# Performance work log

Measured on AMD Instinct MI355X. Metric: run time of the kernel, lower is better.

Reference implementation:

```python
import jax, jax.numpy as jnp
import numpy as np

# DynamicMaskHead config (CondLaneHead defaults, head_layers=3, channels=64)
N, INS_PER_IMG, C, H, W = 4, 8, 64, 160, 256
CIN = C + 2  # coords concatenated
L1, L2, L3 = (C + 2) * C, C * C, C * 1  # weight_nums = [4224, 4096, 64]
B1, B2, B3 = C, C, 1                     # bias_nums   = [64, 64, 1]
NUM_PARAMS = L1 + L2 + L3 + B1 + B2 + B3  # 8513
MASK_BIAS_SHIFT = 2.19  # subtracted from last bias when is_mask=True


def setup_inputs() -> dict:
    key = jax.random.key(0)
    k1, k2 = jax.random.split(key)
    x = jax.random.normal(k1, (N, C, H, W), dtype=jnp.float32)
    mask_head_params = jax.random.normal(k2, (N * INS_PER_IMG, NUM_PARAMS), dtype=jnp.float32) * 0.05
    num_ins = np.full((N,), INS_PER_IMG, dtype=np.int32)  # static per-image instance counts
    return {"x": x, "mask_head_params": mask_head_params, "num_ins": num_ins}


def _locations(h, w, dtype):
    # compute_locations with stride=1: +stride//2 == +0; original normalization
    # (locations[:0], locations[:1]) is a no-op slice, so coords stay unnormalized.
    loc_x = jnp.broadcast_to(jnp.arange(w, dtype=dtype)[None, :], (h, w))
    loc_y = jnp.broadcast_to(jnp.arange(h, dtype=dtype)[:, None], (h, w))
    return jnp.stack([loc_x, loc_y], axis=0)  # [2, H, W]


def reference(x, mask_head_params, num_ins):
    n, _, h, w = x.shape
    loc = _locations(h, w, x.dtype)
    xa = jnp.concatenate([jnp.broadcast_to(loc[None], (n, 2, h, w)), x], axis=1)  # [N, 66, H, W]

    # replicate each image's features per instance (grouped-conv input)
    img_idx = np.repeat(np.arange(n), np.asarray(num_ins))  # static
    num_insts = img_idx.shape[0]
    feats = xa[img_idx].reshape(num_insts, CIN, h * w)  # [I, 66, L]

    # parse_dynamic_params: split flat params into per-instance 1x1 conv weights/biases
    splits = jnp.split(mask_head_params, np.cumsum([L1, L2, L3, B1, B2]), axis=1)
    w0 = splits[0].reshape(num_insts, C, CIN)
    w1 = splits[1].reshape(num_insts, C, C)
    w2 = splits[2].reshape(num_insts, 1, C)
    b0 = splits[3]
    b1 = splits[4]
    b2 = splits[5] - MASK_BIAS_SHIFT  # is_mask=True

    # grouped 1x1 convs == per-instance small matmuls (batched GEMM)
    hdn = jax.nn.relu(jnp.einsum('ioc,icl->iol', w0, feats) + b0[:, :, None])
    hdn = jax.nn.relu(jnp.einsum('ioc,icl->iol', w1, hdn) + b1[:, :, None])
    out = jnp.einsum('ioc,icl->iol', w2, hdn) + b2[:, :, None]  # [I, 1, L]
    return out.reshape(1, num_insts, h, w)
```

## Files before the change

kernel.cpp:

```cpp
#include <hip/hip_runtime.h>
#include <hip/hip_bf16.h>


#define NP 8513
#define HW 40960
#define ISTRIDE 18432
#define OFF_W1 8192
#define OFF_VEC 16384

typedef __attribute__((ext_vector_type(8))) short bf16x8;
typedef __attribute__((ext_vector_type(4))) float f32x4;

__device__ inline unsigned short f2bf(float f) {
  union { float f; unsigned u; } v; v.f = f;
  unsigned r = v.u + 0x7fffu + ((v.u >> 16) & 1u);
  return (unsigned short)(r >> 16);
}
__device__ inline unsigned pk2(float a, float b) {
  __hip_bfloat162 h = __float22bfloat162_rn(float2{a, b});
  union { __hip_bfloat162 h; unsigned u; } v; v.h = h;
  return v.u;
}
__device__ inline void gld16(const void* g, void* l) {
  __builtin_amdgcn_global_load_lds(
      (const __attribute__((address_space(1))) unsigned*)g,
      (__attribute__((address_space(3))) unsigned*)l, 16, 0, 0);
}

__global__ void condlane_prep(const float* __restrict__ params,
                              char* __restrict__ ws) {
  const int inst = blockIdx.x >> 1, part = blockIdx.x & 1;
  const float* __restrict__ p = params + inst * NP;
  char* base = ws + inst * ISTRIDE;
  const int t = threadIdx.x;
  if (part == 0) {
    unsigned short* dst = (unsigned short*)base;
#pragma unroll
    for (int it = 0; it < 16; it++) {
      const int e = it * 256 + t;
      const int frag = e >> 9, lane = (e >> 3) & 63, j = e & 7;
      const int m = (frag >> 1) * 16 + (lane & 15);
      const int k = (frag & 1) * 32 + ((lane >> 4) << 3) + j;
      dst[e] = f2bf(p[m * 66 + 2 + k]);
    }
  } else {
    unsigned short* dst = (unsigned short*)(base + OFF_W1);
#pragma unroll
    for (int it = 0; it < 16; it++) {
      const int e = it * 256 + t;
      const int frag = e >> 9, lane = (e >> 3) & 63, j = e & 7;
      const int m = (frag >> 1) * 16 + (lane & 15);
      const int k = (frag & 1) * 32 + ((lane >> 4) << 3) + j;
      dst[e] = f2bf(p[4224 + m * 64 + k]);
    }
    float* vec = (float*)(base + OFF_VEC);
    if (t < 64) {
      vec[t]       = p[8384 + t];
      vec[64 + t]  = p[t * 66];
      vec[128 + t] = p[t * 66 + 1];
      vec[192 + t] = p[8448 + t];
      vec[256 + t] = p[8320 + t];
    } else if (t == 64) vec[320] = p[8512] - 2.19f;
  }
}

__global__ __launch_bounds__(256, 3) void condlane_main(
    const float* __restrict__ x, const char* __restrict__ ws,
    float* __restrict__ out) {
  __shared__ __align__(16) char smem[53248];
  const int img = blockIdx.y, bx = blockIdx.x;
  const int tid = threadIdx.x, lane = tid & 63, wave = tid >> 6;
  const int col = lane & 15, q = lane >> 4, sw = col & 7;
  const char* const wsb = ws + img * 8 * ISTRIDE;

  auto dma = [&](int i, char* buf) {
    const char* src = wsb + i * ISTRIDE;
#pragma unroll
    for (int u = 0; u < 4; u++) {
      const int off = (wave * 4 + u) * 1024;
      gld16(src + off + lane * 16, buf + off);
    }
    if (wave < 2) {
      const int off = OFF_VEC + wave * 1024;
      gld16(src + off + lane * 16, buf + off);
    }
  };
  dma(0, smem);

  bf16x8 bfr[2][2];
  {
    const float* gx = x + img * 64 * HW + bx * 128 + wave * 32;
#pragma unroll
    for (int nt = 0; nt < 2; nt++)
#pragma unroll
      for (int ks = 0; ks < 2; ks++) {
        float f[8];
#pragma unroll
        for (int j = 0; j < 8; j++)
          f[j] = gx[(ks * 32 + q * 8 + j) * HW + nt * 16 + col];
        union { bf16x8 v; unsigned d[4]; } u;
#pragma unroll
        for (int jj = 0; jj < 4; jj++) u.d[jj] = pk2(f[2 * jj], f[2 * jj + 1]);
        bfr[nt][ks] = u.v;
      }
  }
  __syncthreads();

  const float fyv = (float)(bx >> 1);
  const float fx0 = (float)((bx & 1) * 128 + wave * 32 + col);
  unsigned short* const hwv = (unsigned short*)(smem + 36864) + wave * 2048;
  float* const outb = out + img * 8 * HW + bx * 128 + wave * 32;

  for (int i = 0; i < 8; i++) {
    char* const wb = smem + (i & 1) * ISTRIDE;
    if (i < 7) dma(i + 1, smem + ((i + 1) & 1) * ISTRIDE);
    const float* const vec = (const float*)(wb + OFF_VEC);

    f32x4 acc[4][2];
#pragma unroll
    for (int mt = 0; mt < 4; mt++) {
      const int ro = mt * 16 + q * 4;
      const f32x4 b0v = *(const f32x4*)(vec + ro);
      const f32x4 wxv = *(const f32x4*)(vec + 64 + ro);
      const f32x4 wyv = *(const f32x4*)(vec + 128 + ro);
      const f32x4 byv = b0v + wyv * fyv;
      acc[mt][0] = byv + wxv * fx0;
      acc[mt][1] = byv + wxv * (fx0 + 16.0f);
    }
#pragma unroll
    for (int mt = 0; mt < 4; mt++) {
      const bf16x8 a0 = *(const bf16x8*)(wb + (mt * 2 + 0) * 1024 + lane * 16);
      const bf16x8 a1 = *(const bf16x8*)(wb + (mt * 2 + 1) * 1024 + lane * 16);
#pragma unroll
      for (int nt = 0; nt < 2; nt++) {
        f32x4 c = __builtin_amdgcn_mfma_f32_16x16x32_bf16(a0, bfr[nt][0],
                                                          acc[mt][nt], 0, 0, 0);
        acc[mt][nt] = __builtin_amdgcn_mfma_f32_16x16x32_bf16(a1, bfr[nt][1],
                                                              c, 0, 0, 0);
      }
    }
#pragma unroll
    for (int nt = 0; nt < 2; nt++)
#pragma unroll
      for (int mt = 0; mt < 4; mt++) {
        const f32x4 v = acc[mt][nt];
        uint2 dd;
        dd.x = pk2(fmaxf(v.x, 0.f), fmaxf(v.y, 0.f));
        dd.y = pk2(fmaxf(v.z, 0.f), fmaxf(v.w, 0.f));
        const int kb = (mt * 2 + (q >> 1)) ^ sw;
        *(uint2*)(hwv + nt * 1024 + col * 64 + (kb << 3) + ((q & 1) << 2)) = dd;
      }
    bf16x8 hbf[2][2];
#pragma unroll
    for (int nt = 0; nt < 2; nt++)
#pragma unroll
      for (int ks = 0; ks < 2; ks++)
        hbf[nt][ks] = *(const bf16x8*)(hwv + nt * 1024 + col * 64 +
                                       (((ks * 4 + q) ^ sw) << 3));

    float s0 = 0.f, s1 = 0.f;
#pragma unroll
    for (int mt = 0; mt < 4; mt++) {
      const bf16x8 a0 = *(const bf16x8*)(wb + OFF_W1 + (mt * 2 + 0) * 1024 + lane * 16);
      const bf16x8 a1 = *(const bf16x8*)(wb + OFF_W1 + (mt * 2 + 1) * 1024 + lane * 16);
      const int ro = mt * 16 + q * 4;
      const f32x4 cb  = *(const f32x4*)(vec + 192 + ro);
      const f32x4 w2v = *(const f32x4*)(vec + 256 + ro);
      f32x4 c0 = __builtin_amdgcn_mfma_f32_16x16x32_bf16(a0, hbf[0][0], cb, 0, 0, 0);
      const f32x4 v0 = __builtin_amdgcn_mfma_f32_16x16x32_bf16(a1, hbf[0][1], c0, 0, 0, 0);
      f32x4 c1 = __builtin_amdgcn_mfma_f32_16x16x32_bf16(a0, hbf[1][0], cb, 0, 0, 0);
      const f32x4 v1 = __builtin_amdgcn_mfma_f32_16x16x32_bf16(a1, hbf[1][1], c1, 0, 0, 0);
      s0 += w2v.x * fmaxf(v0.x, 0.f) + w2v.y * fmaxf(v0.y, 0.f) +
            w2v.z * fmaxf(v0.z, 0.f) + w2v.w * fmaxf(v0.w, 0.f);
      s1 += w2v.x * fmaxf(v1.x, 0.f) + w2v.y * fmaxf(v1.y, 0.f) +
            w2v.z * fmaxf(v1.z, 0.f) + w2v.w * fmaxf(v1.w, 0.f);
    }
    const float b2i = vec[320];
    s0 += __shfl_xor(s0, 16, 64); s0 += __shfl_xor(s0, 32, 64);
    s1 += __shfl_xor(s1, 16, 64); s1 += __shfl_xor(s1, 32, 64);
    if (lane < 32)
      outb[i * HW + q * 16 + col] = (q ? s1 : s0) + b2i;

    if (i < 7) __syncthreads();
  }
}

extern "C" void kernel_launch(void* const* d_in, const int* in_sizes, int n_in,
                              void* d_out, int out_size, void* d_ws, size_t ws_size,
                              hipStream_t stream) {
  const float* x      = (const float*)d_in[0];
  const float* params = (const float*)d_in[1];
  float* out = (float*)d_out;

  condlane_prep<<<64, 256, 0, stream>>>(params, (char*)d_ws);
  condlane_main<<<dim3(320, 4), 256, 0, stream>>>(x, (const char*)d_ws, out);
}
```

Measured before the change: 113.2 us.

## Fold layer-0 bias and coords into an extra MFMA, read W1 from global

```diff
diff --git a/kernel.cpp b/kernel.cpp
--- a/kernel.cpp
+++ b/kernel.cpp
@@ -4,9 +4,10 @@
 
 #define NP 8513
 #define HW 40960
-#define ISTRIDE 18432
-#define OFF_W1 8192
-#define OFF_VEC 16384
+#define ISTRIDE 21504
+#define OFF_VEC 12288
+#define OFF_W1 13312
+#define DMABYTES 13312
 
 typedef __attribute__((ext_vector_type(8))) short bf16x8;
 typedef __attribute__((ext_vector_type(4))) float f32x4;
@@ -15,6 +16,10 @@
   union { float f; unsigned u; } v; v.f = f;
   unsigned r = v.u + 0x7fffu + ((v.u >> 16) & 1u);
   return (unsigned short)(r >> 16);
+}
+__device__ inline float bf2f(unsigned short b) {
+  union { unsigned u; float f; } v; v.u = ((unsigned)b) << 16;
+  return v.f;
 }
 __device__ inline unsigned pk2(float a, float b) {
   __hip_bfloat162 h = __float22bfloat162_rn(float2{a, b});
@@ -36,13 +41,27 @@
   if (part == 0) {
     unsigned short* dst = (unsigned short*)base;
 #pragma unroll
-    for (int it = 0; it < 16; it++) {
+    for (int it = 0; it < 24; it++) {
       const int e = it * 256 + t;
       const int frag = e >> 9, lane = (e >> 3) & 63, j = e & 7;
-      const int m = (frag >> 1) * 16 + (lane & 15);
-      const int k = (frag & 1) * 32 + ((lane >> 4) << 3) + j;
-      dst[e] = f2bf(p[m * 66 + 2 + k]);
-    }
+      const int mt = frag / 3, kst = frag % 3;
+      const int m = mt * 16 + (lane & 15);
+      const int kl = ((lane >> 4) << 3) + j;
+      unsigned short bv;
+      if (kst < 2) bv = f2bf(p[m * 66 + 2 + kst * 32 + kl]);
+      else if (kl == 0) bv = f2bf(p[8384 + m]);
+      else if (kl == 1) bv = f2bf(p[m * 66]);
+      else if (kl == 2) { float w = p[m * 66];     bv = f2bf(w - bf2f(f2bf(w))); }
+      else if (kl == 3) bv = f2bf(p[m * 66 + 1]);
+      else if (kl == 4) { float w = p[m * 66 + 1]; bv = f2bf(w - bf2f(f2bf(w))); }
+      else if (kl == 5) { float w = p[8384 + m];   bv = f2bf(w - bf2f(f2bf(w))); }
+      else bv = 0;
+      dst[e] = bv;
+    }
+    float* vec = (float*)(base + OFF_VEC);
+    if (t < 64) { vec[t] = p[8448 + t]; vec[64 + t] = p[8320 + t]; }
+    else if (t == 64) vec[128] = p[8512] - 2.19f;
+    else if (t >= 65 && t < 128) vec[64 + t] = 0.f;
   } else {
     unsigned short* dst = (unsigned short*)(base + OFF_W1);
 #pragma unroll
@@ -53,21 +72,13 @@
       const int k = (frag & 1) * 32 + ((lane >> 4) << 3) + j;
       dst[e] = f2bf(p[4224 + m * 64 + k]);
     }
-    float* vec = (float*)(base + OFF_VEC);
-    if (t < 64) {
-      vec[t]       = p[8384 + t];
-      vec[64 + t]  = p[t * 66];
-      vec[128 + t] = p[t * 66 + 1];
-      vec[192 + t] = p[8448 + t];
-      vec[256 + t] = p[8320 + t];
-    } else if (t == 64) vec[320] = p[8512] - 2.19f;
   }
 }
 
 __global__ __launch_bounds__(256, 3) void condlane_main(
     const float* __restrict__ x, const char* __restrict__ ws,
     float* __restrict__ out) {
-  __shared__ __align__(16) char smem[53248];
+  __shared__ __align__(16) char smem[34816];
   const int img = blockIdx.y, bx = blockIdx.x;
   const int tid = threadIdx.x, lane = tid & 63, wave = tid >> 6;
   const int col = lane & 15, q = lane >> 4, sw = col & 7;
@@ -76,14 +87,12 @@
   auto dma = [&](int i, char* buf) {
     const char* src = wsb + i * ISTRIDE;
 #pragma unroll
-    for (int u = 0; u < 4; u++) {
-      const int off = (wave * 4 + u) * 1024;
+    for (int u = 0; u < 3; u++) {
+      const int off = (wave * 3 + u) * 1024;
       gld16(src + off + lane * 16, buf + off);
     }
-    if (wave < 2) {
-      const int off = OFF_VEC + wave * 1024;
-      gld16(src + off + lane * 16, buf + off);
-    }
+    if (wave == 3 && lane < 48)
+      gld16(src + OFF_VEC + lane * 16, buf + OFF_VEC);
   };
   dma(0, smem);
 
@@ -104,43 +113,52 @@
         bfr[nt][ks] = u.v;
       }
   }
+  bf16x8 baug[2];
+  {
+    const unsigned short fyb = f2bf((float)(bx >> 1));
+#pragma unroll
+    for (int nt = 0; nt < 2; nt++) {
+      const unsigned short fxb =
+          f2bf((float)((bx & 1) * 128 + wave * 32 + nt * 16 + col));
+      union { bf16x8 v; unsigned short s[8]; } u;
+      u.s[0] = (q == 0) ? (unsigned short)0x3F80 : (unsigned short)0;
+      u.s[1] = (q == 0) ? fxb : (unsigned short)0;
+      u.s[2] = u.s[1];
+      u.s[3] = (q == 0) ? fyb : (unsigned short)0;
+      u.s[4] = u.s[3];
+      u.s[5] = u.s[0];
+      u.s[6] = 0; u.s[7] = 0;
+      baug[nt] = u.v;
+    }
+  }
   __syncthreads();
 
-  const float fyv = (float)(bx >> 1);
-  const float fx0 = (float)((bx & 1) * 128 + wave * 32 + col);
-  unsigned short* const hwv = (unsigned short*)(smem + 36864) + wave * 2048;
+  unsigned short* const hwv = (unsigned short*)(smem + 26624) + wave * 1024;
   float* const outb = out + img * 8 * HW + bx * 128 + wave * 32;
+  const f32x4 z4 = {0.f, 0.f, 0.f, 0.f};
 
   for (int i = 0; i < 8; i++) {
-    char* const wb = smem + (i & 1) * ISTRIDE;
-    if (i < 7) dma(i + 1, smem + ((i + 1) & 1) * ISTRIDE);
+    char* const wb = smem + (i & 1) * DMABYTES;
+    if (i < 7) dma(i + 1, smem + ((i + 1) & 1) * DMABYTES);
     const float* const vec = (const float*)(wb + OFF_VEC);
+    const char* const w1g = wsb + i * ISTRIDE + OFF_W1;
 
     f32x4 acc[4][2];
 #pragma unroll
     for (int mt = 0; mt < 4; mt++) {
-      const int ro = mt * 16 + q * 4;
-      const f32x4 b0v = *(const f32x4*)(vec + ro);
-      const f32x4 wxv = *(const f32x4*)(vec + 64 + ro);
-      const f32x4 wyv = *(const f32x4*)(vec + 128 + ro);
-      const f32x4 byv = b0v + wyv * fyv;
-      acc[mt][0] = byv + wxv * fx0;
-      acc[mt][1] = byv + wxv * (fx0 + 16.0f);
-    }
-#pragma unroll
-    for (int mt = 0; mt < 4; mt++) {
-      const bf16x8 a0 = *(const bf16x8*)(wb + (mt * 2 + 0) * 1024 + lane * 16);
-      const bf16x8 a1 = *(const bf16x8*)(wb + (mt * 2 + 1) * 1024 + lane * 16);
+      const bf16x8 a0 = *(const bf16x8*)(wb + (mt * 3 + 0) * 1024 + lane * 16);
+      const bf16x8 a1 = *(const bf16x8*)(wb + (mt * 3 + 1) * 1024 + lane * 16);
+      const bf16x8 a2 = *(const bf16x8*)(wb + (mt * 3 + 2) * 1024 + lane * 16);
 #pragma unroll
       for (int nt = 0; nt < 2; nt++) {
-        f32x4 c = __builtin_amdgcn_mfma_f32_16x16x32_bf16(a0, bfr[nt][0],
-                                                          acc[mt][nt], 0, 0, 0);
-        acc[mt][nt] = __builtin_amdgcn_mfma_f32_16x16x32_bf16(a1, bfr[nt][1],
-                                                              c, 0, 0, 0);
+        f32x4 c = __builtin_amdgcn_mfma_f32_16x16x32_bf16(a0, bfr[nt][0], z4, 0, 0, 0);
+        c = __builtin_amdgcn_mfma_f32_16x16x32_bf16(a1, bfr[nt][1], c, 0, 0, 0);
+        acc[mt][nt] = __builtin_amdgcn_mfma_f32_16x16x32_bf16(a2, baug[nt], c, 0, 0, 0);
       }
     }
-#pragma unroll
-    for (int nt = 0; nt < 2; nt++)
+    bf16x8 hbf[2][2];
+#pragma unroll
+    for (int nt = 0; nt < 2; nt++) {
 #pragma unroll
       for (int mt = 0; mt < 4; mt++) {
         const f32x4 v = acc[mt][nt];
@@ -148,24 +166,20 @@
         dd.x = pk2(fmaxf(v.x, 0.f), fmaxf(v.y, 0.f));
         dd.y = pk2(fmaxf(v.z, 0.f), fmaxf(v.w, 0.f));
         const int kb = (mt * 2 + (q >> 1)) ^ sw;
-        *(uint2*)(hwv + nt * 1024 + col * 64 + (kb << 3) + ((q & 1) << 2)) = dd;
+        *(uint2*)(hwv + col * 64 + (kb << 3) + ((q & 1) << 2)) = dd;
       }
-    bf16x8 hbf[2][2];
-#pragma unroll
-    for (int nt = 0; nt < 2; nt++)
 #pragma unroll
       for (int ks = 0; ks < 2; ks++)
-        hbf[nt][ks] = *(const bf16x8*)(hwv + nt * 1024 + col * 64 +
-                                       (((ks * 4 + q) ^ sw) << 3));
-
+        hbf[nt][ks] = *(const bf16x8*)(hwv + col * 64 + (((ks * 4 + q) ^ sw) << 3));
+    }
     float s0 = 0.f, s1 = 0.f;
 #pragma unroll
     for (int mt = 0; mt < 4; mt++) {
-      const bf16x8 a0 = *(const bf16x8*)(wb + OFF_W1 + (mt * 2 + 0) * 1024 + lane * 16);
-      const bf16x8 a1 = *(const bf16x8*)(wb + OFF_W1 + (mt * 2 + 1) * 1024 + lane * 16);
+      const bf16x8 a0 = *(const bf16x8*)(w1g + (mt * 2 + 0) * 1024 + lane * 16);
+      const bf16x8 a1 = *(const bf16x8*)(w1g + (mt * 2 + 1) * 1024 + lane * 16);
       const int ro = mt * 16 + q * 4;
-      const f32x4 cb  = *(const f32x4*)(vec + 192 + ro);
-      const f32x4 w2v = *(const f32x4*)(vec + 256 + ro);
+      const f32x4 cb  = *(const f32x4*)(vec + ro);
+      const f32x4 w2v = *(const f32x4*)(vec + 64 + ro);
       f32x4 c0 = __builtin_amdgcn_mfma_f32_16x16x32_bf16(a0, hbf[0][0], cb, 0, 0, 0);
       const f32x4 v0 = __builtin_amdgcn_mfma_f32_16x16x32_bf16(a1, hbf[0][1], c0, 0, 0, 0);
       f32x4 c1 = __builtin_amdgcn_mfma_f32_16x16x32_bf16(a0, hbf[1][0], cb, 0, 0, 0);
@@ -175,7 +189,7 @@
       s1 += w2v.x * fmaxf(v1.x, 0.f) + w2v.y * fmaxf(v1.y, 0.f) +
             w2v.z * fmaxf(v1.z, 0.f) + w2v.w * fmaxf(v1.w, 0.f);
     }
-    const float b2i = vec[320];
+    const float b2i = vec[128];
     s0 += __shfl_xor(s0, 16, 64); s0 += __shfl_xor(s0, 32, 64);
     s1 += __shfl_xor(s1, 16, 64); s1 += __shfl_xor(s1, 32, 64);
     if (lane < 32)
```

After: 118.8 us. +4.9%, slower.
